# Performance work log

Hardware: AMD Instinct MI355X
Metric: run time of the kernel (lower is better)

Reference implementation:

```python
import jax, jax.numpy as jnp
import numpy as np

ALPHA = 0.5

def setup_inputs() -> dict:
    key = jax.random.key(0)
    k1, k2 = jax.random.split(key)
    B, S, F_IN, F_OUT = 64, 512, 1024, 1024
    x = jax.random.normal(k1, (B, S, F_IN), dtype=jnp.float32)
    W = jax.random.normal(k2, (F_OUT, F_IN), dtype=jnp.float32) * (F_IN ** -0.5)
    return {"x": x, "W": W}

def reference(x, W):
    # x: [B, S, F_in], W: [F_out, F_in] (torch Linear layout, no bias)
    alpha = jnp.asarray(ALPHA, dtype=x.dtype)
    # Project all segments at once (the big GEMM), then scan the EMA recurrence.
    y = jnp.einsum('bsf,of->bso', x, W)  # [B, S, F_out]
    y_t = jnp.swapaxes(y, 0, 1)          # [S, B, F_out] for scan over segments

    def step(h, yk):
        h = alpha * h + (1 - alpha) * yk
        return h, h

    h0 = jnp.zeros((x.shape[0], W.shape[0]), dtype=x.dtype)
    hk, hiddens_t = jax.lax.scan(step, h0, y_t)
    hiddens = jnp.swapaxes(hiddens_t, 0, 1)  # [B, S, F_out]
    return (hk, hiddens)
```

## Files before the change

### kernel.cpp

```cpp
#include <hip/hip_runtime.h>
#include <hip/hip_bf16.h>
#include <stdint.h>

#define B_DIM 64
#define S_DIM 512
#define K_DIM 1024
#define N_DIM 1024
#define M_DIM (B_DIM * S_DIM)
#define N_TILES 256

typedef __attribute__((ext_vector_type(8))) short short8;
typedef __attribute__((ext_vector_type(4))) float floatx4;

__device__ __forceinline__ uint4 pack8_bf16(float4 a, float4 b) {
  union { unsigned short u[8]; uint4 q; } pk;
  __hip_bfloat16 t;
  t = __float2bfloat16(a.x); pk.u[0] = *(unsigned short*)&t;
  t = __float2bfloat16(a.y); pk.u[1] = *(unsigned short*)&t;
  t = __float2bfloat16(a.z); pk.u[2] = *(unsigned short*)&t;
  t = __float2bfloat16(a.w); pk.u[3] = *(unsigned short*)&t;
  t = __float2bfloat16(b.x); pk.u[4] = *(unsigned short*)&t;
  t = __float2bfloat16(b.y); pk.u[5] = *(unsigned short*)&t;
  t = __float2bfloat16(b.z); pk.u[6] = *(unsigned short*)&t;
  t = __float2bfloat16(b.w); pk.u[7] = *(unsigned short*)&t;
  return pk.q;
}

__global__ __launch_bounds__(256) void conv_x_kernel(
    const float* __restrict__ x, __hip_bfloat16* __restrict__ xs) {
  const size_t stride = 2048u * 256u;
  size_t t = (size_t)blockIdx.x * 256 + threadIdx.x;
  #pragma unroll
  for (int it = 0; it < 8; ++it, t += stride) {
    float4 v0 = *(const float4*)(x + t * 8);
    float4 v1 = *(const float4*)(x + t * 8 + 4);
    *(uint4*)(xs + t * 8) = pack8_bf16(v0, v1);
  }
}

__global__ __launch_bounds__(256) void conv_w_kernel(
    const float* __restrict__ W, __hip_bfloat16* __restrict__ Wb) {
  const size_t t = (size_t)blockIdx.x * 256 + threadIdx.x;
  float4 v0 = *(const float4*)(W + t * 8);
  float4 v1 = *(const float4*)(W + t * 8 + 4);
  *(uint4*)(Wb + t * 8) = pack8_bf16(v0, v1);
}

__global__ __launch_bounds__(256) void wx_kernel(
    const float* __restrict__ x, __hip_bfloat16* __restrict__ wx) {
  const int t = blockIdx.x;
  const int b = t >> 2;
  const int c = t & 3;
  const int k4 = threadIdx.x * 4;
  float4 acc = {0.f, 0.f, 0.f, 0.f};
  if (c != 0) {
    const float* base = x + ((size_t)b * S_DIM + c * 128) * K_DIM + k4;
    float wgt = 0.5f;
    #pragma unroll
    for (int j = 1; j <= 16; ++j) {
      float4 v = *(const float4*)(base - (size_t)j * K_DIM);
      acc.x += wgt * v.x; acc.y += wgt * v.y;
      acc.z += wgt * v.z; acc.w += wgt * v.w;
      wgt *= 0.5f;
    }
  }
  union { unsigned short u[4]; uint2 q; } pk;
  __hip_bfloat16 h;
  h = __float2bfloat16(acc.x); pk.u[0] = *(unsigned short*)&h;
  h = __float2bfloat16(acc.y); pk.u[1] = *(unsigned short*)&h;
  h = __float2bfloat16(acc.z); pk.u[2] = *(unsigned short*)&h;
  h = __float2bfloat16(acc.w); pk.u[3] = *(unsigned short*)&h;
  *(uint2*)(wx + (size_t)t * K_DIM + k4) = pk.q;
}

template <bool MAIN>
__global__ __launch_bounds__(256) void gemm_tmpl(
    const __hip_bfloat16* __restrict__ A,
    const __hip_bfloat16* __restrict__ Bw,
    float* __restrict__ out,
    const float* __restrict__ warm) {
  __shared__ __hip_bfloat16 lA[128 * 64];
  __shared__ __hip_bfloat16 lB[128 * 64];
  __shared__ float hbuf[128];

  const int tid  = threadIdx.x;
  const int lane = tid & 63;
  const int w    = tid >> 6;
  const int wm   = (w >> 1) * 64;
  const int wn   = (w & 1) * 64;
  const int quad = lane >> 4;
  const int l15  = lane & 15;
  const int r7   = l15 & 7;

  int m0, n0;
  if (MAIN) {
    const int bi    = blockIdx.x;
    const int xcd   = bi & 7;
    const int local = bi >> 3;
    m0 = (xcd * 32 + (local >> 3)) * 128;
    n0 = (local & 7) * 128;
  } else {
    m0 = (blockIdx.x >> 3) * 128;
    n0 = (blockIdx.x & 7) * 128;
  }

  floatx4 acc[4][4] = {};

  for (int k0 = 0; k0 < K_DIM; k0 += 64) {
    #pragma unroll
    for (int p = 0; p < 4; ++p) {
      int c    = tid + p * 256;
      int r    = c >> 3;
      int slot = c & 7;
      int kc   = (slot ^ (r & 7)) * 8;
      const __hip_bfloat16* ga = A  + (size_t)(m0 + r) * K_DIM + k0 + kc;
      const __hip_bfloat16* gb = Bw + (size_t)(n0 + r) * K_DIM + k0 + kc;
      __builtin_amdgcn_global_load_lds(
          (const __attribute__((address_space(1))) void*)ga,
          (__attribute__((address_space(3))) void*)&lA[c * 8], 16, 0, 0);
      __builtin_amdgcn_global_load_lds(
          (const __attribute__((address_space(1))) void*)gb,
          (__attribute__((address_space(3))) void*)&lB[c * 8], 16, 0, 0);
    }
    __syncthreads();

    #pragma unroll
    for (int kk = 0; kk < 64; kk += 32) {
      const int q0 = kk >> 3;
      short8 af[4], bfr[4];
      #pragma unroll
      for (int i = 0; i < 4; ++i) {
        af[i]  = *(const short8*)&lA[(wm + i * 16 + l15) * 64 +
                                     (((q0 + quad) ^ r7) * 8)];
        bfr[i] = *(const short8*)&lB[(wn + i * 16 + l15) * 64 +
                                     (((q0 + quad) ^ r7) * 8)];
      }
      #pragma unroll
      for (int i = 0; i < 4; ++i)
        #pragma unroll
        for (int j = 0; j < 4; ++j)
          acc[i][j] = __builtin_amdgcn_mfma_f32_16x16x32_bf16(
              af[i], bfr[j], acc[i][j], 0, 0, 0);
    }
    __syncthreads();
  }

  if (MAIN) {
    const float fq = (quad == 0) ? 1.f : (quad == 1) ? 0.0625f
                   : (quad == 2) ? 0.00390625f : 2.44140625e-4f;
    const int tile = m0 >> 7;
    #pragma unroll
    for (int j = 0; j < 4; ++j) {
      const int colIdx = wn + j * 16 + l15;
      float Wst = 0.f;
      if (w < 2) Wst = warm[(size_t)tile * N_DIM + n0 + colIdx];
      #pragma unroll
      for (int i = 0; i < 4; ++i) {
        const float y0 = acc[i][j][0], y1 = acc[i][j][1];
        const float y2 = acc[i][j][2], y3 = acc[i][j][3];
        const float L0 = 0.5f * y0;
        const float L1 = 0.5f * (L0 + y1);
        const float L2 = 0.5f * (L1 + y2);
        const float L3 = 0.5f * (L2 + y3);
        float P = L3;
        float t1 = __shfl_up(P, 16);
        if (quad >= 1) P += 0.0625f * t1;
        float t2 = __shfl_up(P, 32);
        if (quad >= 2) P += 0.00390625f * t2;
        float H = __shfl_up(P, 16);
        H = (quad >= 1) ? H : 0.f;
        const float S = H + fq * Wst;
        acc[i][j][0] = L0 + 0.5f    * S;
        acc[i][j][1] = L1 + 0.25f   * S;
        acc[i][j][2] = L2 + 0.125f  * S;
        acc[i][j][3] = L3 + 0.0625f * S;
        const float F = __shfl(P, 48 + l15);
        Wst = F + 1.52587890625e-05f * Wst;
      }
      if (w < 2 && quad == 0) hbuf[colIdx] = Wst;
    }
    __syncthreads();
    if (w >= 2) {
      #pragma unroll
      for (int j = 0; j < 4; ++j) {
        const float Z = hbuf[wn + j * 16 + l15] * fq;
        #pragma unroll
        for (int i = 0; i < 4; ++i) {
          const float fi = (i == 0) ? 1.f
                         : (i == 1) ? 1.52587890625e-05f
                         : (i == 2) ? 2.3283064365386963e-10f
                                    : 3.552713678800501e-15f;
          const float base = fi * Z;
          acc[i][j][0] += 0.5f    * base;
          acc[i][j][1] += 0.25f   * base;
          acc[i][j][2] += 0.125f  * base;
          acc[i][j][3] += 0.0625f * base;
        }
      }
    }
  }

  float* hid = MAIN ? out + B_DIM * N_DIM : out;
  #pragma unroll
  for (int i = 0; i < 4; ++i) {
    #pragma unroll
    for (int j = 0; j < 4; ++j) {
      #pragma unroll
      for (int r = 0; r < 4; ++r) {
        int gm = m0 + wm + i * 16 + quad * 4 + r;
        int gn = n0 + wn + j * 16 + l15;
        float v = acc[i][j][r];
        hid[(size_t)gm * N_DIM + gn] = v;
        if (MAIN && ((gm & (S_DIM - 1)) == (S_DIM - 1))) {
          out[(size_t)(gm >> 9) * N_DIM + gn] = v;
        }
      }
    }
  }
}

extern "C" void kernel_launch(void* const* d_in, const int* in_sizes, int n_in,
                              void* d_out, int out_size, void* d_ws, size_t ws_size,
                              hipStream_t stream) {
  const float* x = (const float*)d_in[0];
  const float* W = (const float*)d_in[1];
  float* out = (float*)d_out;

  __hip_bfloat16* xs = (__hip_bfloat16*)d_ws;
  __hip_bfloat16* Wb = xs + (size_t)M_DIM * K_DIM;
  __hip_bfloat16* wx = Wb + (size_t)N_DIM * K_DIM;
  float*          wy = (float*)(wx + (size_t)N_TILES * K_DIM);

  conv_x_kernel<<<dim3(2048), dim3(256), 0, stream>>>(x, xs);
  conv_w_kernel<<<dim3((N_DIM * K_DIM) / (256 * 8)), dim3(256), 0, stream>>>(W, Wb);
  wx_kernel<<<dim3(N_TILES), dim3(256), 0, stream>>>(x, wx);
  gemm_tmpl<false><<<dim3(16), dim3(256), 0, stream>>>(wx, Wb, wy, nullptr);
  gemm_tmpl<true><<<dim3((M_DIM / 128) * (N_DIM / 128)), dim3(256), 0, stream>>>(xs, Wb, out, wy);
}
```

Measured before the change: 344.1 us.

## Fuse x bf16 conversion into main GEMM A-tile loads and merge prep kernels

Drops the separate pass that converts all of x to bf16. The main GEMM now reads fp32 x directly, converts it in registers and writes the swizzled bf16 tile into LDS. The W conversion and the warm-state kernels are merged into one launch. This removes a full write and re-read of a 64MB bf16 copy of x and two launches. In exchange, each x tile is re-read as fp32 by all 8 column blocks, and the A-tile loads become synchronous register loads instead of direct-to-LDS loads.

```diff
diff --git a/kernel.cpp b/kernel.cpp
--- a/kernel.cpp
+++ b/kernel.cpp
@@ -26,56 +26,44 @@
   return pk.q;
 }
 
-__global__ __launch_bounds__(256) void conv_x_kernel(
-    const float* __restrict__ x, __hip_bfloat16* __restrict__ xs) {
-  const size_t stride = 2048u * 256u;
-  size_t t = (size_t)blockIdx.x * 256 + threadIdx.x;
-  #pragma unroll
-  for (int it = 0; it < 8; ++it, t += stride) {
-    float4 v0 = *(const float4*)(x + t * 8);
-    float4 v1 = *(const float4*)(x + t * 8 + 4);
-    *(uint4*)(xs + t * 8) = pack8_bf16(v0, v1);
-  }
-}
-
-__global__ __launch_bounds__(256) void conv_w_kernel(
-    const float* __restrict__ W, __hip_bfloat16* __restrict__ Wb) {
-  const size_t t = (size_t)blockIdx.x * 256 + threadIdx.x;
-  float4 v0 = *(const float4*)(W + t * 8);
-  float4 v1 = *(const float4*)(W + t * 8 + 4);
-  *(uint4*)(Wb + t * 8) = pack8_bf16(v0, v1);
-}
-
-__global__ __launch_bounds__(256) void wx_kernel(
+__global__ __launch_bounds__(256) void prep_kernel(
+    const float* __restrict__ W, __hip_bfloat16* __restrict__ Wb,
     const float* __restrict__ x, __hip_bfloat16* __restrict__ wx) {
-  const int t = blockIdx.x;
-  const int b = t >> 2;
-  const int c = t & 3;
-  const int k4 = threadIdx.x * 4;
-  float4 acc = {0.f, 0.f, 0.f, 0.f};
-  if (c != 0) {
-    const float* base = x + ((size_t)b * S_DIM + c * 128) * K_DIM + k4;
-    float wgt = 0.5f;
-    #pragma unroll
-    for (int j = 1; j <= 16; ++j) {
-      float4 v = *(const float4*)(base - (size_t)j * K_DIM);
-      acc.x += wgt * v.x; acc.y += wgt * v.y;
-      acc.z += wgt * v.z; acc.w += wgt * v.w;
-      wgt *= 0.5f;
-    }
-  }
-  union { unsigned short u[4]; uint2 q; } pk;
-  __hip_bfloat16 h;
-  h = __float2bfloat16(acc.x); pk.u[0] = *(unsigned short*)&h;
-  h = __float2bfloat16(acc.y); pk.u[1] = *(unsigned short*)&h;
-  h = __float2bfloat16(acc.z); pk.u[2] = *(unsigned short*)&h;
-  h = __float2bfloat16(acc.w); pk.u[3] = *(unsigned short*)&h;
-  *(uint2*)(wx + (size_t)t * K_DIM + k4) = pk.q;
+  if (blockIdx.x < 512) {
+    const size_t t = (size_t)blockIdx.x * 256 + threadIdx.x;
+    float4 v0 = *(const float4*)(W + t * 8);
+    float4 v1 = *(const float4*)(W + t * 8 + 4);
+    *(uint4*)(Wb + t * 8) = pack8_bf16(v0, v1);
+  } else {
+    const int t = blockIdx.x - 512;
+    const int b = t >> 2;
+    const int c = t & 3;
+    const int k4 = threadIdx.x * 4;
+    float4 acc = {0.f, 0.f, 0.f, 0.f};
+    if (c != 0) {
+      const float* base = x + ((size_t)b * S_DIM + c * 128) * K_DIM + k4;
+      float wgt = 0.5f;
+      #pragma unroll
+      for (int j = 1; j <= 16; ++j) {
+        float4 v = *(const float4*)(base - (size_t)j * K_DIM);
+        acc.x += wgt * v.x; acc.y += wgt * v.y;
+        acc.z += wgt * v.z; acc.w += wgt * v.w;
+        wgt *= 0.5f;
+      }
+    }
+    union { unsigned short u[4]; uint2 q; } pk;
+    __hip_bfloat16 h;
+    h = __float2bfloat16(acc.x); pk.u[0] = *(unsigned short*)&h;
+    h = __float2bfloat16(acc.y); pk.u[1] = *(unsigned short*)&h;
+    h = __float2bfloat16(acc.z); pk.u[2] = *(unsigned short*)&h;
+    h = __float2bfloat16(acc.w); pk.u[3] = *(unsigned short*)&h;
+    *(uint2*)(wx + (size_t)t * K_DIM + k4) = pk.q;
+  }
 }
 
 template <bool MAIN>
 __global__ __launch_bounds__(256) void gemm_tmpl(
-    const __hip_bfloat16* __restrict__ A,
+    const void* __restrict__ Aptr,
     const __hip_bfloat16* __restrict__ Bw,
     float* __restrict__ out,
     const float* __restrict__ warm) {
@@ -113,14 +101,36 @@
       int r    = c >> 3;
       int slot = c & 7;
       int kc   = (slot ^ (r & 7)) * 8;
-      const __hip_bfloat16* ga = A  + (size_t)(m0 + r) * K_DIM + k0 + kc;
       const __hip_bfloat16* gb = Bw + (size_t)(n0 + r) * K_DIM + k0 + kc;
-      __builtin_amdgcn_global_load_lds(
-          (const __attribute__((address_space(1))) void*)ga,
-          (__attribute__((address_space(3))) void*)&lA[c * 8], 16, 0, 0);
       __builtin_amdgcn_global_load_lds(
           (const __attribute__((address_space(1))) void*)gb,
           (__attribute__((address_space(3))) void*)&lB[c * 8], 16, 0, 0);
+    }
+    if constexpr (MAIN) {
+      const float* Af = (const float*)Aptr;
+      #pragma unroll
+      for (int p = 0; p < 4; ++p) {
+        int c = tid + p * 256;
+        int r = c >> 3;
+        int q = c & 7;
+        const float* ga = Af + (size_t)(m0 + r) * K_DIM + k0 + q * 8;
+        float4 v0 = *(const float4*)ga;
+        float4 v1 = *(const float4*)(ga + 4);
+        *(uint4*)&lA[r * 64 + ((q ^ (r & 7)) * 8)] = pack8_bf16(v0, v1);
+      }
+    } else {
+      const __hip_bfloat16* Ab = (const __hip_bfloat16*)Aptr;
+      #pragma unroll
+      for (int p = 0; p < 4; ++p) {
+        int c    = tid + p * 256;
+        int r    = c >> 3;
+        int slot = c & 7;
+        int kc   = (slot ^ (r & 7)) * 8;
+        const __hip_bfloat16* ga = Ab + (size_t)(m0 + r) * K_DIM + k0 + kc;
+        __builtin_amdgcn_global_load_lds(
+            (const __attribute__((address_space(1))) void*)ga,
+            (__attribute__((address_space(3))) void*)&lA[c * 8], 16, 0, 0);
+      }
     }
     __syncthreads();
 
@@ -226,14 +236,11 @@
   const float* W = (const float*)d_in[1];
   float* out = (float*)d_out;
 
-  __hip_bfloat16* xs = (__hip_bfloat16*)d_ws;
-  __hip_bfloat16* Wb = xs + (size_t)M_DIM * K_DIM;
+  __hip_bfloat16* Wb = (__hip_bfloat16*)d_ws;
   __hip_bfloat16* wx = Wb + (size_t)N_DIM * K_DIM;
   float*          wy = (float*)(wx + (size_t)N_TILES * K_DIM);
 
-  conv_x_kernel<<<dim3(2048), dim3(256), 0, stream>>>(x, xs);
-  conv_w_kernel<<<dim3((N_DIM * K_DIM) / (256 * 8)), dim3(256), 0, stream>>>(W, Wb);
-  wx_kernel<<<dim3(N_TILES), dim3(256), 0, stream>>>(x, wx);
+  prep_kernel<<<dim3(768), dim3(256), 0, stream>>>(W, Wb, x, wx);
   gemm_tmpl<false><<<dim3(16), dim3(256), 0, stream>>>(wx, Wb, wy, nullptr);
-  gemm_tmpl<true><<<dim3((M_DIM / 128) * (N_DIM / 128)), dim3(256), 0, stream>>>(xs, Wb, out, wy);
-}
+  gemm_tmpl<true><<<dim3((M_DIM / 128) * (N_DIM / 128)), dim3(256), 0, stream>>>(x, Wb, out, wy);
+}
```

Result: slower. 366.1 us (+6.4%).
